# Optimization experiments

Hardware: AMD Instinct MI355X
Metric: run time of the kernel (lower is better)

Reference implementation:

```python
import jax, jax.numpy as jnp
import numpy as np

D_K = 64
TAU = 1.0
THRESHOLD = 0.5


def setup_inputs() -> dict:
    key = jax.random.key(0)
    k1, k2, k3 = jax.random.split(key, 3)
    B, N, F = 32, 512, 320
    F_OBS = 256
    h = jax.random.normal(k1, (B, N, F), dtype=jnp.float32)
    # xavier_uniform with gain 1.414 on (F_OBS, D_K)
    limit = float(1.414 * np.sqrt(6.0 / (F_OBS + D_K)))
    a_link = jax.random.uniform(k2, (F_OBS, D_K), minval=-limit, maxval=limit, dtype=jnp.float32)
    b_link = jax.random.uniform(k3, (F_OBS, D_K), minval=-limit, maxval=limit, dtype=jnp.float32)
    return {"h": h, "a_link": a_link, "b_link": b_link, "rollout": 1}


def reference(h, a_link, b_link, rollout):
    F_OBS = a_link.shape[0]
    # original detaches the sliced features
    hx = jax.lax.stop_gradient(h[:, :, :F_OBS])
    h_i = jnp.einsum('bik,kl->bil', hx, a_link)
    h_j = jnp.einsum('bjk,kl->bjl', hx, b_link)
    logits = jnp.einsum('bil,bjl->bij', h_i, h_j) / jnp.sqrt(jnp.float32(D_K))

    # gumbel_sigmoid with rollout=True: no noise, just sigmoid(logits/tau)
    y_soft = jax.nn.sigmoid(logits / TAU)
    y_hard = (y_soft > THRESHOLD).astype(y_soft.dtype)
    # straight-through estimator
    A = y_hard - jax.lax.stop_gradient(y_soft) + y_soft

    B, N, _ = logits.shape
    eye_b = jnp.eye(N, dtype=bool)[None]          # [1, N, N]
    eye_f = jnp.eye(N, dtype=y_soft.dtype)[None]  # [1, N, N]

    # log-prob of the sampled hard edges, off-diagonal entries only
    sel = A * y_soft + (1.0 - A) * (1.0 - y_soft)
    logp = jnp.log(sel + 1e-8)
    probs = jnp.sum(jnp.where(eye_b, 0.0, logp), axis=(1, 2))  # [B]

    # zero the diagonal of A, then add identity (vectorized form of the per-batch diag loop)
    A_out = A - A * eye_f + eye_f
    # .squeeze(0) is a no-op for B > 1
    return A_out, probs
```

## Files before the change

### kernel.cpp

```cpp
#include <hip/hip_runtime.h>
#include <math.h>

#define BATCH   32
#define NPTS    512
#define FDIM    320
#define FOBS    256
#define DK      64
#define MROWS   (BATCH * NPTS)
#define A_ELEMS ((size_t)BATCH * NPTS * NPTS)

typedef __bf16  bf16x8 __attribute__((ext_vector_type(8)));
typedef float   f32x4  __attribute__((ext_vector_type(4)));
typedef ushort  u16x8  __attribute__((ext_vector_type(8)));

__device__ __forceinline__ ushort f2bf(float f) {
    unsigned u = __builtin_bit_cast(unsigned, f);
    return (ushort)((u + 0x7fffu + ((u >> 16) & 1u)) >> 16);
}

__device__ __forceinline__ bf16x8 ld_bf8(const ushort* p) {
    return __builtin_bit_cast(bf16x8, *reinterpret_cast<const uint4*>(p));
}

__global__ __launch_bounds__(256) void k1_proj(const float* __restrict__ h,
                                               const float* __restrict__ al,
                                               const float* __restrict__ bl,
                                               ushort* __restrict__ hi,
                                               ushort* __restrict__ hj) {
    __shared__ float a_lds[32][36];
    __shared__ float w_lds[32][132];

    const int t  = threadIdx.x;
    const int m0 = blockIdx.x * 32;
    const int ty = t >> 4, tx = t & 15;

    float acc[2][8];
#pragma unroll
    for (int i = 0; i < 2; ++i)
#pragma unroll
        for (int j = 0; j < 8; ++j) acc[i][j] = 0.f;

    for (int k0 = 0; k0 < FOBS; k0 += 32) {
        __syncthreads();
        {
            int r = t >> 3, q = t & 7;
            float4 v = *reinterpret_cast<const float4*>(
                &h[(size_t)(m0 + r) * FDIM + k0 + q * 4]);
            *reinterpret_cast<float4*>(&a_lds[r][q * 4]) = v;
        }
#pragma unroll
        for (int s = 0; s < 4; ++s) {
            int id = t + s * 256;
            int kk = id >> 5, ch = id & 31;
            const float* src = (ch < 16) ? &al[(size_t)(k0 + kk) * 64 + ch * 4]
                                         : &bl[(size_t)(k0 + kk) * 64 + (ch - 16) * 4];
            float4 v = *reinterpret_cast<const float4*>(src);
            *reinterpret_cast<float4*>(&w_lds[kk][ch * 4]) = v;
        }
        __syncthreads();

#pragma unroll
        for (int kk = 0; kk < 32; kk += 4) {
            float a_k[2][4];
#pragma unroll
            for (int i = 0; i < 2; ++i) {
                float4 v = *reinterpret_cast<const float4*>(&a_lds[ty * 2 + i][kk]);
                a_k[i][0] = v.x; a_k[i][1] = v.y; a_k[i][2] = v.z; a_k[i][3] = v.w;
            }
#pragma unroll
            for (int q = 0; q < 4; ++q) {
                float4 w0 = *reinterpret_cast<const float4*>(&w_lds[kk + q][tx * 8]);
                float4 w1 = *reinterpret_cast<const float4*>(&w_lds[kk + q][tx * 8 + 4]);
                float wv[8] = {w0.x, w0.y, w0.z, w0.w, w1.x, w1.y, w1.z, w1.w};
#pragma unroll
                for (int i = 0; i < 2; ++i) {
                    float a = a_k[i][q];
#pragma unroll
                    for (int j = 0; j < 8; ++j)
                        acc[i][j] = fmaf(a, wv[j], acc[i][j]);
                }
            }
        }
    }

    const int c = tx * 8;
    ushort* dst = (c < 64) ? (hi + c) : (hj + (c - 64));
#pragma unroll
    for (int i = 0; i < 2; ++i) {
        size_t row = (size_t)(m0 + ty * 2 + i);
        u16x8 v;
#pragma unroll
        for (int j = 0; j < 8; ++j) v[j] = f2bf(acc[i][j]);
        *reinterpret_cast<u16x8*>(&dst[row * 64]) = v;
    }
}

__global__ __launch_bounds__(256, 4) void k2_mfma(const ushort* __restrict__ hi,
                                                  const ushort* __restrict__ hj,
                                                  float* __restrict__ Aout,
                                                  float* __restrict__ partials) {
    __shared__ float red[4];
    const int t  = threadIdx.x;
    const int w  = t >> 6;
    const int l  = t & 63;
    const int lr = l & 15;
    const int lg = l >> 4;
    const int jt = blockIdx.x, it = blockIdx.y, b = blockIdx.z;
    const int i0 = it * 64, j0 = jt * 64;

    const ushort* hib = hi + ((size_t)b * NPTS + i0) * DK;
    const ushort* hjb = hj + ((size_t)b * NPTS + j0) * DK;

    bf16x8 afr[2];
#pragma unroll
    for (int ks = 0; ks < 2; ++ks)
        afr[ks] = ld_bf8(&hib[(size_t)(16 * w + lr) * DK + ks * 32 + lg * 8]);

    bf16x8 bfr[4][2];
#pragma unroll
    for (int jtt = 0; jtt < 4; ++jtt)
#pragma unroll
        for (int ks = 0; ks < 2; ++ks)
            bfr[jtt][ks] = ld_bf8(&hjb[(size_t)(16 * jtt + lr) * DK + ks * 32 + lg * 8]);

    f32x4 acc[4];
#pragma unroll
    for (int jtt = 0; jtt < 4; ++jtt) acc[jtt] = (f32x4){0.f, 0.f, 0.f, 0.f};

#pragma unroll
    for (int ks = 0; ks < 2; ++ks)
#pragma unroll
        for (int jtt = 0; jtt < 4; ++jtt)
            acc[jtt] = __builtin_amdgcn_mfma_f32_16x16x32_bf16(
                afr[ks], bfr[jtt][ks], acc[jtt], 0, 0, 0);

    float lsum = 0.f;
    const int drow0 = i0 + 16 * w + lg * 4;
#pragma unroll
    for (int jtt = 0; jtt < 4; ++jtt) {
        const int col = j0 + 16 * jtt + lr;
#pragma unroll
        for (int r = 0; r < 4; ++r) {
            const int row = drow0 + r;
            float x  = acc[jtt][r] * 0.125f;
            float ax = fabsf(x);
            float nl = __logf(1.0f + __expf(-ax));
            bool diag = (row == col);
            float ov = (diag || x > 0.f) ? 1.f : 0.f;
            if (!diag) lsum -= nl;
            Aout[((size_t)b * NPTS + row) * NPTS + col] = ov;
        }
    }

#pragma unroll
    for (int off = 32; off > 0; off >>= 1) lsum += __shfl_down(lsum, off);
    if (l == 0) red[w] = lsum;
    __syncthreads();
    if (t == 0) {
        float s = (red[0] + red[1]) + (red[2] + red[3]);
        partials[(size_t)b * 64 + it * 8 + jt] = s;
    }
}

__global__ __launch_bounds__(64) void k3_reduce(const float* __restrict__ partials,
                                                float* __restrict__ probs) {
    int b = blockIdx.x;
    float s = partials[(size_t)b * 64 + threadIdx.x];
#pragma unroll
    for (int off = 32; off > 0; off >>= 1) s += __shfl_down(s, off);
    if (threadIdx.x == 0) probs[b] = s;
}

extern "C" void kernel_launch(void* const* d_in, const int* in_sizes, int n_in,
                              void* d_out, int out_size, void* d_ws, size_t ws_size,
                              hipStream_t stream) {
    const float* h  = (const float*)d_in[0];
    const float* al = (const float*)d_in[1];
    const float* bl = (const float*)d_in[2];
    float* out = (float*)d_out;

    ushort* hi      = (ushort*)d_ws;
    ushort* hj      = hi + (size_t)MROWS * DK;
    float* partials = (float*)(hj + (size_t)MROWS * DK);

    k1_proj<<<MROWS / 32, 256, 0, stream>>>(h, al, bl, hi, hj);

    dim3 g2(NPTS / 64, NPTS / 64, BATCH);
    k2_mfma<<<g2, 256, 0, stream>>>(hi, hj, out, partials);

    k3_reduce<<<BATCH, 64, 0, stream>>>(partials, out + A_ELEMS);
}
```

Before: 44.81 us.

## Use bf16 MFMA for projection, remap k2 block order, nontemporal A stores

The FP32 LDS-tiled projection GEMM becomes a bf16 MFMA kernel. A small pre-kernel transposes the weights into a bf16 buffer, and the h rows are converted to bf16 in registers. The attention kernel gets a flattened grid with a swizzled block-to-batch mapping and writes A with nontemporal stores to avoid polluting cache with the large output. The changes add an extra launch and lower the projection to bf16 precision, which could flip signs of near-zero logits.

```diff
diff --git a/kernel.cpp b/kernel.cpp
--- a/kernel.cpp
+++ b/kernel.cpp
@@ -22,76 +22,63 @@
     return __builtin_bit_cast(bf16x8, *reinterpret_cast<const uint4*>(p));
 }
 
-__global__ __launch_bounds__(256) void k1_proj(const float* __restrict__ h,
-                                               const float* __restrict__ al,
-                                               const float* __restrict__ bl,
+__global__ __launch_bounds__(256) void k0_wt(const float* __restrict__ al,
+                                             const float* __restrict__ bl,
+                                             ushort* __restrict__ wt) {
+    const int n = blockIdx.x;
+    const int k = threadIdx.x;
+    const float* src = (n < 64) ? al : bl;
+    const int nn = n & 63;
+    wt[(size_t)n * FOBS + k] = f2bf(src[(size_t)k * DK + nn]);
+}
+
+__global__ __launch_bounds__(256) void k1_mfma(const float* __restrict__ h,
+                                               const ushort* __restrict__ wt,
                                                ushort* __restrict__ hi,
                                                ushort* __restrict__ hj) {
-    __shared__ float a_lds[32][36];
-    __shared__ float w_lds[32][132];
+    const int t  = threadIdx.x;
+    const int w  = t >> 6;
+    const int l  = t & 63;
+    const int lr = l & 15;
+    const int lg = l >> 4;
+    const int rb = blockIdx.x * 32 + 16 * (w & 1);
+    const int cb = 64 * (w >> 1);
 
-    const int t  = threadIdx.x;
-    const int m0 = blockIdx.x * 32;
-    const int ty = t >> 4, tx = t & 15;
+    const float* hrow = h + (size_t)(rb + lr) * FDIM;
+    bf16x8 afr[8];
+#pragma unroll
+    for (int ks = 0; ks < 8; ++ks) {
+        const float* p = hrow + ks * 32 + lg * 8;
+        float4 v0 = *reinterpret_cast<const float4*>(p);
+        float4 v1 = *reinterpret_cast<const float4*>(p + 4);
+        u16x8 u;
+        u[0] = f2bf(v0.x); u[1] = f2bf(v0.y); u[2] = f2bf(v0.z); u[3] = f2bf(v0.w);
+        u[4] = f2bf(v1.x); u[5] = f2bf(v1.y); u[6] = f2bf(v1.z); u[7] = f2bf(v1.w);
+        afr[ks] = __builtin_bit_cast(bf16x8, u);
+    }
 
-    float acc[2][8];
+    f32x4 acc[4];
 #pragma unroll
-    for (int i = 0; i < 2; ++i)
-#pragma unroll
-        for (int j = 0; j < 8; ++j) acc[i][j] = 0.f;
-
-    for (int k0 = 0; k0 < FOBS; k0 += 32) {
-        __syncthreads();
-        {
-            int r = t >> 3, q = t & 7;
-            float4 v = *reinterpret_cast<const float4*>(
-                &h[(size_t)(m0 + r) * FDIM + k0 + q * 4]);
-            *reinterpret_cast<float4*>(&a_lds[r][q * 4]) = v;
-        }
-#pragma unroll
-        for (int s = 0; s < 4; ++s) {
-            int id = t + s * 256;
-            int kk = id >> 5, ch = id & 31;
-            const float* src = (ch < 16) ? &al[(size_t)(k0 + kk) * 64 + ch * 4]
-                                         : &bl[(size_t)(k0 + kk) * 64 + (ch - 16) * 4];
-            float4 v = *reinterpret_cast<const float4*>(src);
-            *reinterpret_cast<float4*>(&w_lds[kk][ch * 4]) = v;
-        }
-        __syncthreads();
+    for (int cf = 0; cf < 4; ++cf) acc[cf] = (f32x4){0.f, 0.f, 0.f, 0.f};
 
 #pragma unroll
-        for (int kk = 0; kk < 32; kk += 4) {
-            float a_k[2][4];
+    for (int ks = 0; ks < 8; ++ks) {
 #pragma unroll
-            for (int i = 0; i < 2; ++i) {
-                float4 v = *reinterpret_cast<const float4*>(&a_lds[ty * 2 + i][kk]);
-                a_k[i][0] = v.x; a_k[i][1] = v.y; a_k[i][2] = v.z; a_k[i][3] = v.w;
-            }
-#pragma unroll
-            for (int q = 0; q < 4; ++q) {
-                float4 w0 = *reinterpret_cast<const float4*>(&w_lds[kk + q][tx * 8]);
-                float4 w1 = *reinterpret_cast<const float4*>(&w_lds[kk + q][tx * 8 + 4]);
-                float wv[8] = {w0.x, w0.y, w0.z, w0.w, w1.x, w1.y, w1.z, w1.w};
-#pragma unroll
-                for (int i = 0; i < 2; ++i) {
-                    float a = a_k[i][q];
-#pragma unroll
-                    for (int j = 0; j < 8; ++j)
-                        acc[i][j] = fmaf(a, wv[j], acc[i][j]);
-                }
-            }
+        for (int cf = 0; cf < 4; ++cf) {
+            bf16x8 bfr = ld_bf8(&wt[(size_t)(cb + 16 * cf + lr) * FOBS + ks * 32 + lg * 8]);
+            acc[cf] = __builtin_amdgcn_mfma_f32_16x16x32_bf16(afr[ks], bfr, acc[cf], 0, 0, 0);
         }
     }
 
-    const int c = tx * 8;
-    ushort* dst = (c < 64) ? (hi + c) : (hj + (c - 64));
+    ushort* dst = (cb == 0) ? hi : hj;
 #pragma unroll
-    for (int i = 0; i < 2; ++i) {
-        size_t row = (size_t)(m0 + ty * 2 + i);
-        u16x8 v;
+    for (int cf = 0; cf < 4; ++cf) {
+        const int nn = 16 * cf + lr;
 #pragma unroll
-        for (int j = 0; j < 8; ++j) v[j] = f2bf(acc[i][j]);
-        *reinterpret_cast<u16x8*>(&dst[row * 64]) = v;
+        for (int r = 0; r < 4; ++r) {
+            const int m = rb + lg * 4 + r;
+            dst[(size_t)m * DK + nn] = f2bf(acc[cf][r]);
+        }
     }
 }
 
@@ -100,12 +87,17 @@
                                                   float* __restrict__ Aout,
                                                   float* __restrict__ partials) {
     __shared__ float red[4];
+    const int id  = blockIdx.x;
+    const int sub = id >> 3;
+    const int b   = (id & 7) * 4 + (sub >> 6);
+    const int it  = (sub >> 3) & 7;
+    const int jt  = sub & 7;
+
     const int t  = threadIdx.x;
     const int w  = t >> 6;
     const int l  = t & 63;
     const int lr = l & 15;
     const int lg = l >> 4;
-    const int jt = blockIdx.x, it = blockIdx.y, b = blockIdx.z;
     const int i0 = it * 64, j0 = jt * 64;
 
     const ushort* hib = hi + ((size_t)b * NPTS + i0) * DK;
@@ -148,7 +140,7 @@
             bool diag = (row == col);
             float ov = (diag || x > 0.f) ? 1.f : 0.f;
             if (!diag) lsum -= nl;
-            Aout[((size_t)b * NPTS + row) * NPTS + col] = ov;
+            __builtin_nontemporal_store(ov, &Aout[((size_t)b * NPTS + row) * NPTS + col]);
         }
     }
 
@@ -181,12 +173,14 @@
 
     ushort* hi      = (ushort*)d_ws;
     ushort* hj      = hi + (size_t)MROWS * DK;
-    float* partials = (float*)(hj + (size_t)MROWS * DK);
+    ushort* wt      = hj + (size_t)MROWS * DK;
+    float* partials = (float*)(wt + 128 * FOBS);
 
-    k1_proj<<<MROWS / 32, 256, 0, stream>>>(h, al, bl, hi, hj);
+    k0_wt<<<128, 256, 0, stream>>>(al, bl, wt);
 
-    dim3 g2(NPTS / 64, NPTS / 64, BATCH);
-    k2_mfma<<<g2, 256, 0, stream>>>(hi, hj, out, partials);
+    k1_mfma<<<MROWS / 32, 256, 0, stream>>>(h, wt, hi, hj);
+
+    k2_mfma<<<(NPTS / 64) * (NPTS / 64) * BATCH, 256, 0, stream>>>(hi, hj, out, partials);
 
     k3_reduce<<<BATCH, 64, 0, stream>>>(partials, out + A_ELEMS);
 }
```

Measured after the change: 38.58 us. 1.16x faster.
